# Kernel optimization log

Measured on AMD Instinct MI355X. Metric: run time of the kernel, lower is better.

Reference implementation:

```python
import math
import jax, jax.numpy as jnp
import numpy as np

H = 8  # num_heads


def setup_inputs() -> dict:
    key = jax.random.key(0)
    ks = jax.random.split(key, 9)
    B, N = 2, 4096
    Cc, C, Cs = 512, 512, 128  # in_channels, hidden_size, in_channels//4
    f = lambda k, shp: jax.random.normal(k, shp, dtype=jnp.float32) * 0.02
    return {
        "s": f(ks[0], (B, N, Cc)),
        "h": f(ks[1], (B, N, Cs)),
        "sh": f(ks[2], (B, N, C)),
        "temperature": jnp.full((H, 1, 1), 0.1, jnp.float32),
        "temperature2": jnp.full((H, 1, 1), 0.1, jnp.float32),
        "Wq_c": f(ks[3], (Cc, Cc)),
        "Wq_s": f(ks[4], (C, C)),
        "Wk_c": f(ks[5], (C, C)),
        "Wv_c": f(ks[6], (C, C)),
        "Wk_s": f(ks[7], (C, C)),
        "Wv_s": f(ks[8], (Cs, Cs)),
    }


def reference(s, h, sh, temperature, temperature2, Wq_c, Wq_s, Wk_c, Wv_c, Wk_s, Wv_s):
    B, N, C = sh.shape
    Cc = s.shape[2]
    Cs = h.shape[2]
    dc, d, ds = Cc // H, C // H, Cs // H

    # torch nn.Linear(bias=False): y = x @ W.T ; reshapes replicate torch's
    # direct reshape(B, H, N, d) layout (no (B,N,H,d)+transpose head split).
    q_c = (s @ Wq_c.T).reshape(B, H, N, dc).swapaxes(-1, -2)  # (B,H,dc,N)
    q_s = (sh @ Wq_s.T).reshape(B, H, N, d)
    k_c = (sh @ Wk_c.T).reshape(B, H, N, d)
    v_c = (sh @ Wv_c.T).reshape(B, H, N, d)
    k_s = (sh @ Wk_s.T).reshape(B, H, N, d)
    v_s = (h @ Wv_s.T).reshape(B, H, N, ds)

    # Channel branch: (B,H,dc,N) @ (B,H,N,d) -> (B,H,dc,d)
    attn_ca = (q_c @ k_c) / math.sqrt(d) * temperature
    attn_ca = jax.nn.softmax(attn_ca, axis=-1)
    x_ca = (attn_ca @ v_c.swapaxes(-2, -1)).reshape(B, N, Cc)  # (B,H,dc,N)->(B,N,Cc)

    # Spatial branch: (B,H,N,d) @ (B,H,d,N) -> (B,H,N,N)
    attn_sa = (q_s @ k_s.swapaxes(-2, -1)) / math.sqrt(d) * temperature2
    attn_sa = jax.nn.softmax(attn_sa, axis=-1)
    x_sa = (attn_sa @ v_s).reshape(B, N, Cs)  # (B,H,N,ds)->(B,N,Cs)

    return jnp.concatenate([x_ca, x_sa], axis=2)  # (B,N,Cc+Cs)
```

## Files before the change

### kernel.cpp

```cpp
#include <hip/hip_runtime.h>


typedef __attribute__((ext_vector_type(8))) __bf16 bf16x8;
typedef __attribute__((ext_vector_type(4))) __bf16 bf16x4;
typedef __attribute__((ext_vector_type(4))) float  f32x4;
typedef __attribute__((ext_vector_type(4))) short  s16x4;

#define LOG2E 1.44269504088896340736f

static __device__ __forceinline__ f32x4 mfma16(bf16x4 a, bf16x4 b, f32x4 c)
{
#if __has_builtin(__builtin_amdgcn_mfma_f32_16x16x16bf16_1k)
    union { bf16x4 h; s16x4 s; } ua, ub;
    ua.h = a; ub.h = b;
    return __builtin_amdgcn_mfma_f32_16x16x16bf16_1k(ua.s, ub.s, c, 0, 0, 0);
#elif __has_builtin(__builtin_amdgcn_mfma_f32_16x16x16_bf16)
    return __builtin_amdgcn_mfma_f32_16x16x16_bf16(a, b, c, 0, 0, 0);
#else
    asm("v_mfma_f32_16x16x16_bf16 %0, %1, %2, %0" : "+v"(c) : "v"(a), "v"(b));
    return c;
#endif
}

__global__ void detect_dtype(const unsigned* __restrict__ temp, int* __restrict__ flag)
{
    if (threadIdx.x == 0) {
        const unsigned w = temp[0];
        flag[0] = ((w >> 16) == (w & 0xffffu)) ? 1 : 0;
    }
}

struct ProjArgs {
    const void* X[6];
    const void* W[6];
    __bf16*     Y[6];
    int         K[6];
    int         yofs[7];
    int         ng;
};

__global__ __launch_bounds__(256) void proj_gemm(ProjArgs args,
                                                 const int* __restrict__ flag)
{
    __shared__ __align__(16) __bf16 As[128][72];
    __shared__ __align__(16) __bf16 Bs[128][72];
    const int bf = *flag;
    const int by = blockIdx.y;
    int g = 0;
    while (by >= args.yofs[g + 1]) ++g;
    const int n0 = (by - args.yofs[g]) * 128;
    const int N  = (args.yofs[g + 1] - args.yofs[g]) * 128;
    const int K  = args.K[g];
    const void* X = args.X[g];
    const void* W = args.W[g];
    __bf16*     Y = args.Y[g];

    const int m0 = blockIdx.x * 128;
    const int t = threadIdx.x;
    const int wave = t >> 6, lane = t & 63;
    const int wr = (wave >> 1) * 64, wc = (wave & 1) * 64;
    const int m16 = lane & 15, quad = lane >> 4;

    f32x4 acc[4][4];
#pragma unroll
    for (int i = 0; i < 4; ++i)
#pragma unroll
        for (int j = 0; j < 4; ++j) acc[i][j] = (f32x4){0.f, 0.f, 0.f, 0.f};

    if (bf) {
        const __bf16* Xb = (const __bf16*)X;
        const __bf16* Wb = (const __bf16*)W;
        bf16x8 pa[4], pb[4];
        auto load = [&](int k0) {
#pragma unroll
            for (int i = 0; i < 4; ++i) {
                const int idx = t + i * 256, row = idx >> 3, off = (idx & 7) * 8;
                pa[i] = *(const bf16x8*)(Xb + (size_t)(m0 + row) * K + k0 + off);
            }
#pragma unroll
            for (int i = 0; i < 4; ++i) {
                const int idx = t + i * 256, row = idx >> 3, off = (idx & 7) * 8;
                pb[i] = *(const bf16x8*)(Wb + (size_t)(n0 + row) * K + k0 + off);
            }
        };
        load(0);
        for (int k0 = 0; k0 < K; k0 += 64) {
            __syncthreads();
#pragma unroll
            for (int i = 0; i < 4; ++i) {
                const int idx = t + i * 256, row = idx >> 3, off = (idx & 7) * 8;
                *(bf16x8*)&As[row][off] = pa[i];
            }
#pragma unroll
            for (int i = 0; i < 4; ++i) {
                const int idx = t + i * 256, row = idx >> 3, off = (idx & 7) * 8;
                *(bf16x8*)&Bs[row][off] = pb[i];
            }
            __syncthreads();
            if (k0 + 64 < K) load(k0 + 64);
#pragma unroll
            for (int kc = 0; kc < 2; ++kc) {
                const int ko = kc * 32 + quad * 8;
                bf16x8 a[4], b[4];
#pragma unroll
                for (int i = 0; i < 4; ++i) a[i] = *(const bf16x8*)&As[wr + i * 16 + m16][ko];
#pragma unroll
                for (int j = 0; j < 4; ++j) b[j] = *(const bf16x8*)&Bs[wc + j * 16 + m16][ko];
#pragma unroll
                for (int i = 0; i < 4; ++i)
#pragma unroll
                    for (int j = 0; j < 4; ++j)
                        acc[i][j] = __builtin_amdgcn_mfma_f32_16x16x32_bf16(a[i], b[j], acc[i][j], 0, 0, 0);
            }
        }
    } else {
        const float* Xf = (const float*)X;
        const float* Wf = (const float*)W;
        f32x4 pa[8], pb[8];
        auto load = [&](int k0) {
#pragma unroll
            for (int i = 0; i < 8; ++i) {
                const int idx = t + i * 256, row = idx >> 4, c = (idx & 15) * 4;
                pa[i] = *(const f32x4*)(Xf + (size_t)(m0 + row) * K + k0 + c);
            }
#pragma unroll
            for (int i = 0; i < 8; ++i) {
                const int idx = t + i * 256, row = idx >> 4, c = (idx & 15) * 4;
                pb[i] = *(const f32x4*)(Wf + (size_t)(n0 + row) * K + k0 + c);
            }
        };
        load(0);
        for (int k0 = 0; k0 < K; k0 += 64) {
            __syncthreads();
#pragma unroll
            for (int i = 0; i < 8; ++i) {
                const int idx = t + i * 256, row = idx >> 4, c = (idx & 15) * 4;
                bf16x4 ha;
#pragma unroll
                for (int e = 0; e < 4; ++e) ha[e] = (__bf16)pa[i][e];
                *(bf16x4*)&As[row][c] = ha;
            }
#pragma unroll
            for (int i = 0; i < 8; ++i) {
                const int idx = t + i * 256, row = idx >> 4, c = (idx & 15) * 4;
                bf16x4 hb;
#pragma unroll
                for (int e = 0; e < 4; ++e) hb[e] = (__bf16)pb[i][e];
                *(bf16x4*)&Bs[row][c] = hb;
            }
            __syncthreads();
            if (k0 + 64 < K) load(k0 + 64);
#pragma unroll
            for (int kc = 0; kc < 2; ++kc) {
                const int ko = kc * 32 + quad * 8;
                bf16x8 a[4], b[4];
#pragma unroll
                for (int i = 0; i < 4; ++i) a[i] = *(const bf16x8*)&As[wr + i * 16 + m16][ko];
#pragma unroll
                for (int j = 0; j < 4; ++j) b[j] = *(const bf16x8*)&Bs[wc + j * 16 + m16][ko];
#pragma unroll
                for (int i = 0; i < 4; ++i)
#pragma unroll
                    for (int j = 0; j < 4; ++j)
                        acc[i][j] = __builtin_amdgcn_mfma_f32_16x16x32_bf16(a[i], b[j], acc[i][j], 0, 0, 0);
            }
        }
    }
#pragma unroll
    for (int i = 0; i < 4; ++i)
#pragma unroll
        for (int j = 0; j < 4; ++j)
#pragma unroll
            for (int r = 0; r < 4; ++r) {
                const int gm = m0 + wr + i * 16 + quad * 4 + r;
                const int gn = n0 + wc + j * 16 + m16;
                Y[(size_t)gm * N + gn] = (__bf16)acc[i][j][r];
            }
}

__global__ __launch_bounds__(256) void zero_f32(float* __restrict__ p, int n)
{
    const int i = blockIdx.x * 256 + threadIdx.x;
    if (i < n) p[i] = 0.f;
}

template <int ATOMIC>
__global__ __launch_bounds__(256) void chan_qk(const __bf16* __restrict__ Qc,
                                               const __bf16* __restrict__ Kc,
                                               float* __restrict__ S)
{
    __shared__ __align__(16) __bf16 Ql[128][72];
    __shared__ __align__(16) __bf16 Kl[128][72];
    const int bx = blockIdx.x;
    const int bh = bx >> 5, split = bx & 31;
    const int b = bh >> 3, hh = bh & 7;
    const int n0 = split * 128;
    const int t = threadIdx.x;
    const size_t base = ((size_t)b * 4096 + (size_t)hh * 512) * 512;

    for (int idx = t; idx < 1024; idx += 256) {
        const int row = idx >> 3, off = (idx & 7) * 8;
        *(bf16x8*)&Ql[row][off] = *(const bf16x8*)(Qc + base + (size_t)(n0 + row) * 64 + off);
        *(bf16x8*)&Kl[row][off] = *(const bf16x8*)(Kc + base + (size_t)(n0 + row) * 64 + off);
    }
    __syncthreads();

    const int ti = t >> 4, tj = t & 15;
    float acc[4][4];
#pragma unroll
    for (int r = 0; r < 4; ++r)
#pragma unroll
        for (int c = 0; c < 4; ++c) acc[r][c] = 0.f;

#pragma unroll 4
    for (int n = 0; n < 128; ++n) {
        bf16x4 qv = *(const bf16x4*)&Ql[n][ti * 4];
        bf16x4 kv = *(const bf16x4*)&Kl[n][tj * 4];
        float qf[4], kf[4];
#pragma unroll
        for (int x = 0; x < 4; ++x) { qf[x] = (float)qv[x]; kf[x] = (float)kv[x]; }
#pragma unroll
        for (int r = 0; r < 4; ++r)
#pragma unroll
            for (int c = 0; c < 4; ++c) acc[r][c] += qf[r] * kf[c];
    }
    if (ATOMIC) {
        float* Sb = S + (size_t)bh * 4096;
#pragma unroll
        for (int r = 0; r < 4; ++r)
#pragma unroll
            for (int c = 0; c < 4; ++c)
                atomicAdd(&Sb[(ti * 4 + r) * 64 + tj * 4 + c], acc[r][c]);
    } else {
        float* Sp = S + (size_t)bx * 4096;
#pragma unroll
        for (int r = 0; r < 4; ++r)
#pragma unroll
            for (int c = 0; c < 4; ++c)
                Sp[(ti * 4 + r) * 64 + tj * 4 + c] = acc[r][c];
    }
}

__global__ __launch_bounds__(256) void qk_reduce(const float* __restrict__ Spart,
                                                 float* __restrict__ S)
{
    const int tid = blockIdx.x * 256 + threadIdx.x;
    const int bh = tid >> 12, ij = tid & 4095;
    const float* p = Spart + (size_t)bh * 32 * 4096 + ij;
    float s = 0.f;
#pragma unroll
    for (int sp = 0; sp < 32; ++sp) s += p[(size_t)sp * 4096];
    S[(size_t)bh * 4096 + ij] = s;
}

__global__ __launch_bounds__(64) void chan_softmax(const float* __restrict__ S,
                                                   const void* __restrict__ temp,
                                                   __bf16* __restrict__ P,
                                                   const int* __restrict__ flag)
{
    const int bh = blockIdx.x;
    const int hh = bh & 7;
    const int i = threadIdx.x;
    const float tv = (*flag) ? (float)((const __bf16*)temp)[hh] : ((const float*)temp)[hh];
    const float scale = 0.125f * tv;
    const float* row = S + (size_t)bh * 4096 + (size_t)i * 64;
    float v[64];
    float mx = -1e30f;
#pragma unroll
    for (int j = 0; j < 64; ++j) { v[j] = row[j] * scale; mx = fmaxf(mx, v[j]); }
    float sum = 0.f;
#pragma unroll
    for (int j = 0; j < 64; ++j) { float e = __builtin_amdgcn_exp2f((v[j] - mx) * LOG2E); v[j] = e; sum += e; }
    const float inv = 1.f / sum;
    __bf16* prow = P + (size_t)bh * 4096 + (size_t)i * 64;
#pragma unroll
    for (int j = 0; j < 64; ++j) prow[j] = (__bf16)(v[j] * inv);
}

__global__ __launch_bounds__(256) void chan_av(const __bf16* __restrict__ P,
                                               const __bf16* __restrict__ Vc,
                                               void* __restrict__ out,
                                               const int* __restrict__ flag)
{
    const int bf = *flag;
    const int bx = blockIdx.x;
    const int bh = bx >> 6, ch = bx & 63;
    const int b = bh >> 3, hh = bh & 7;
    const int n0 = ch * 64;
    const int t = threadIdx.x, wave = t >> 6, lane = t & 63;
    const int m16 = lane & 15, quad = lane >> 4;
    const size_t base = ((size_t)b * 4096 + (size_t)hh * 512) * 512;
    const __bf16* Pb = P + (size_t)bh * 4096;

    bf16x8 a[2];
#pragma unroll
    for (int kc = 0; kc < 2; ++kc)
        a[kc] = *(const bf16x8*)(Pb + (wave * 16 + m16) * 64 + kc * 32 + quad * 8);

    f32x4 acc[4];
#pragma unroll
    for (int nt = 0; nt < 4; ++nt) {
        acc[nt] = (f32x4){0.f, 0.f, 0.f, 0.f};
        const int n = n0 + nt * 16 + m16;
        bf16x8 bv[2];
#pragma unroll
        for (int kc = 0; kc < 2; ++kc)
            bv[kc] = *(const bf16x8*)(Vc + base + (size_t)n * 64 + kc * 32 + quad * 8);
#pragma unroll
        for (int kc = 0; kc < 2; ++kc)
            acc[nt] = __builtin_amdgcn_mfma_f32_16x16x32_bf16(a[kc], bv[kc], acc[nt], 0, 0, 0);
    }

#pragma unroll
    for (int nt = 0; nt < 4; ++nt) {
        const int n = n0 + nt * 16 + m16;
#pragma unroll
        for (int r = 0; r < 4; ++r) {
            const int i = wave * 16 + quad * 4 + r;
            const size_t addr = (size_t)b * 2621440
                              + (size_t)(hh * 512 + i * 8 + (n >> 9)) * 640 + (n & 511);
            if (bf) ((__bf16*)out)[addr] = (__bf16)acc[nt][r];
            else    ((float*)out)[addr]  = acc[nt][r];
        }
    }
}

template <int PATH>
__global__ __launch_bounds__(512) void flash_sa(const __bf16* __restrict__ Qs,
                                                const __bf16* __restrict__ Ks,
                                                const __bf16* __restrict__ Vs,
                                                const void* __restrict__ temp2,
                                                void* __restrict__ out,
                                                float* __restrict__ po,
                                                float* __restrict__ pl,
                                                const int* __restrict__ flag)
{
    __shared__ __align__(16) __bf16 Kl[2][64][72];
    __shared__ __align__(16) __bf16 Vt[2][16][72];
    const int bf = *flag;
    const int bid = blockIdx.x;
    const int qt = bid & 15;
    const int bh = bid >> 4;
    const int b = bh >> 3, hh = bh & 7;
    const int nspl = gridDim.y;
    const int spl  = blockIdx.y;
    const int nkt  = 64 / nspl;
    const int kt0  = spl * nkt;
    const int t = threadIdx.x, wave = t >> 6, lane = t & 63;
    const int m16 = lane & 15, quad = lane >> 4;
    const size_t base  = ((size_t)b * 4096 + (size_t)hh * 512) * 512;
    const size_t vbase = ((size_t)b * 4096 + (size_t)hh * 512) * 128;
    const float tv = bf ? (float)((const __bf16*)temp2)[hh] : ((const float*)temp2)[hh];
    const float sl = 0.125f * tv * LOG2E;

    bf16x8 qa[2][2];
#pragma unroll
    for (int g = 0; g < 2; ++g) {
        const int qrow = qt * 256 + g * 128 + wave * 16 + m16;
#pragma unroll
        for (int kc = 0; kc < 2; ++kc) {
            bf16x8 raw = *(const bf16x8*)(Qs + base + (size_t)qrow * 64 + kc * 32 + quad * 8);
#pragma unroll
            for (int e = 0; e < 8; ++e) qa[g][kc][e] = (__bf16)((float)raw[e] * sl);
        }
    }

    bf16x4 ones;
#pragma unroll
    for (int e = 0; e < 4; ++e) ones[e] = (__bf16)1.0f;

    const int krow = t >> 3, koff = (t & 7) * 8;
    const bool vact = t < 256;
    const int vrow = t & 63, vcq = (t >> 6) & 3;
    bf16x8 pk;
    bf16x4 pv;
    auto pref = [&](int kt) {
        pk = *(const bf16x8*)(Ks + base + (size_t)(kt * 64 + krow) * 64 + koff);
        if (vact) pv = *(const bf16x4*)(Vs + vbase + (size_t)(kt * 64 + vrow) * 16 + vcq * 4);
    };
    auto stage = [&](int bi) {
        *(bf16x8*)&Kl[bi][krow][koff] = pk;
        if (vact) {
#pragma unroll
            for (int e = 0; e < 4; ++e) Vt[bi][vcq * 4 + e][vrow] = pv[e];
        }
    };

    pref(kt0);
    stage(0);
    pref(kt0 + 1);
    __syncthreads();

    f32x4 o[2]  = {(f32x4){0.f, 0.f, 0.f, 0.f}, (f32x4){0.f, 0.f, 0.f, 0.f}};
    f32x4 o2[2] = {(f32x4){0.f, 0.f, 0.f, 0.f}, (f32x4){0.f, 0.f, 0.f, 0.f}};

    for (int kk = 0; kk < nkt; ++kk) {
        const int cur = kk & 1;

        bf16x8 kb[4][2];
        bf16x4 vb16[4];
#pragma unroll
        for (int ct = 0; ct < 4; ++ct)
#pragma unroll
            for (int kc = 0; kc < 2; ++kc)
                kb[ct][kc] = *(const bf16x8*)&Kl[cur][ct * 16 + m16][kc * 32 + quad * 8];
#pragma unroll
        for (int ct = 0; ct < 4; ++ct)
            vb16[ct] = *(const bf16x4*)&Vt[cur][m16][ct * 16 + quad * 4];

        if (kk + 1 < nkt) stage(cur ^ 1);
        if (kk + 2 < nkt) pref(kt0 + kk + 2);

#pragma unroll
        for (int g = 0; g < 2; ++g) {
            f32x4 st[4];
#pragma unroll
            for (int ct = 0; ct < 4; ++ct) {
                st[ct] = (f32x4){0.f, 0.f, 0.f, 0.f};
#pragma unroll
                for (int kc = 0; kc < 2; ++kc)
                    st[ct] = __builtin_amdgcn_mfma_f32_16x16x32_bf16(kb[ct][kc], qa[g][kc], st[ct], 0, 0, 0);
            }
#pragma unroll
            for (int ct = 0; ct < 4; ++ct) {
                bf16x4 pe;
#pragma unroll
                for (int r = 0; r < 4; ++r)
                    pe[r] = (__bf16)__builtin_amdgcn_exp2f(st[ct][r]);
                o[g]  = mfma16(pe, vb16[ct], o[g]);
                o2[g] = mfma16(pe, ones,     o2[g]);
            }
        }
        __syncthreads();
    }

    asm volatile("s_nop 7\n\ts_nop 7");

    if (nspl == 1) {
#pragma unroll
        for (int g = 0; g < 2; ++g) {
#pragma unroll
            for (int r = 0; r < 4; ++r) {
                const int n = qt * 256 + g * 128 + wave * 16 + quad * 4 + r;
                const float val = o[g][r] / o2[g][r];
                const size_t addr = (size_t)b * 2621440
                                  + (size_t)(hh * 512 + (n >> 3)) * 640 + 512 + (n & 7) * 16 + m16;
                if (bf) ((__bf16*)out)[addr] = (__bf16)val;
                else    ((float*)out)[addr]  = val;
            }
        }
    } else {
#pragma unroll
        for (int g = 0; g < 2; ++g) {
#pragma unroll
            for (int r = 0; r < 4; ++r) {
                const int n = qt * 256 + g * 128 + wave * 16 + quad * 4 + r;
                const size_t rowi = ((size_t)spl * 16 + bh) * 4096 + n;
                po[rowi * 16 + m16] = o[g][r];
                if (m16 == 0) pl[rowi] = o2[g][r];
            }
        }
    }
}

__global__ __launch_bounds__(256) void flash_combine(const float* __restrict__ po,
                                                     const float* __restrict__ pl,
                                                     void* __restrict__ out,
                                                     const int* __restrict__ flag,
                                                     int nspl)
{
    const int bf = *flag;
    const int tid = blockIdx.x * 256 + threadIdx.x;
    const int bh = tid >> 12, n = tid & 4095;
    const int b = bh >> 3, hh = bh & 7;

    float acc[16];
#pragma unroll
    for (int c = 0; c < 16; ++c) acc[c] = 0.f;
    float l = 0.f;
    for (int sp = 0; sp < nspl; ++sp) {
        const size_t rowi = ((size_t)sp * 16 + bh) * 4096 + n;
        const f32x4* r = (const f32x4*)(po + rowi * 16);
#pragma unroll
        for (int q = 0; q < 4; ++q) {
            const f32x4 v = r[q];
#pragma unroll
            for (int e = 0; e < 4; ++e) acc[q * 4 + e] += v[e];
        }
        l += pl[rowi];
    }
    const float inv = 1.f / l;
    const size_t addr = (size_t)b * 2621440
                      + (size_t)(hh * 512 + (n >> 3)) * 640 + 512 + (n & 7) * 16;
    if (bf) {
#pragma unroll
        for (int c = 0; c < 16; ++c) ((__bf16*)out)[addr + c] = (__bf16)(acc[c] * inv);
    } else {
#pragma unroll
        for (int c = 0; c < 16; ++c) ((float*)out)[addr + c] = acc[c] * inv;
    }
}

extern "C" void kernel_launch(void* const* d_in, const int* in_sizes, int n_in,
                              void* d_out, int out_size, void* d_ws, size_t ws_size,
                              hipStream_t stream)
{
    const void* s    = d_in[0];
    const void* h_   = d_in[1];
    const void* sh   = d_in[2];
    const void* t1   = d_in[3];
    const void* t2   = d_in[4];
    const void* Wq_c = d_in[5];
    const void* Wq_s = d_in[6];
    const void* Wk_c = d_in[7];
    const void* Wv_c = d_in[8];
    const void* Wk_s = d_in[9];
    const void* Wv_s = d_in[10];

    const dim3 blk(256);
    const size_t PROJ = 4194304;

    const size_t WIDE_BYTES = 5 * PROJ * 2 + 1048576 * 2 + 65536 * 4 + 65536 * 2 + 256;

    if (ws_size >= WIDE_BYTES) {
        __bf16* qc = (__bf16*)d_ws;
        __bf16* kc = qc + PROJ;
        __bf16* vc = kc + PROJ;
        __bf16* qs = vc + PROJ;
        __bf16* ks = qs + PROJ;
        __bf16* vs = ks + PROJ;
        float*  Sb = (float*)(vs + 1048576);
        __bf16* Pb = (__bf16*)(Sb + 65536);
        int*  flag = (int*)(Pb + 65536);

        detect_dtype<<<dim3(1), dim3(64), 0, stream>>>((const unsigned*)t1, flag);

        ProjArgs pa{};
        const void* Xs[6] = {s, sh, sh, sh, sh, h_};
        const void* Ws[6] = {Wq_c, Wk_c, Wv_c, Wq_s, Wk_s, Wv_s};
        __bf16*     Ys[6] = {qc, kc, vc, qs, ks, vs};
        const int   Ks_[6] = {512, 512, 512, 512, 512, 128};
        const int   yt[6] = {4, 4, 4, 4, 4, 1};
        pa.ng = 6;
        int ofs = 0;
        for (int g = 0; g < 6; ++g) {
            pa.X[g] = Xs[g]; pa.W[g] = Ws[g]; pa.Y[g] = Ys[g]; pa.K[g] = Ks_[g];
            pa.yofs[g] = ofs; ofs += yt[g];
        }
        pa.yofs[6] = ofs;

        proj_gemm<<<dim3(64, 21), blk, 0, stream>>>(pa, flag);

        zero_f32<<<dim3(256), blk, 0, stream>>>(Sb, 65536);
        chan_qk<1><<<dim3(512), blk, 0, stream>>>(qc, kc, Sb);
        chan_softmax<<<dim3(16), dim3(64), 0, stream>>>(Sb, t1, Pb, flag);
        chan_av<<<dim3(1024), blk, 0, stream>>>(Pb, vc, d_out, flag);
        float* po = (float*)qc;
        float* pl = po + 4ull * 1048576;
        flash_sa<0><<<dim3(256, 4), dim3(512), 0, stream>>>(qs, ks, vs, t2, d_out, po, pl, flag);
        flash_combine<<<dim3(256), blk, 0, stream>>>(po, pl, d_out, flag, 4);
    } else {
        __bf16* A  = (__bf16*)d_ws;
        __bf16* Bf = A + PROJ;
        __bf16* D  = Bf + PROJ;
        float*  Sb = (float*)(D + 1048576);
        __bf16* Pb = (__bf16*)(Sb + 65536);
        int*  flag = (int*)(Pb + 65536);

        detect_dtype<<<dim3(1), dim3(64), 0, stream>>>((const unsigned*)t1, flag);

        auto mk2 = [&](const void* X0, const void* W0, __bf16* Y0, int K0, int t0,
                       const void* X1, const void* W1, __bf16* Y1, int K1, int t1_) {
            ProjArgs p{};
            p.ng = 2;
            p.X[0] = X0; p.W[0] = W0; p.Y[0] = Y0; p.K[0] = K0;
            p.X[1] = X1; p.W[1] = W1; p.Y[1] = Y1; p.K[1] = K1;
            p.yofs[0] = 0; p.yofs[1] = t0; p.yofs[2] = t0 + t1_;
            return p;
        };

        const size_t fb_end = (size_t)((char*)(flag + 1) - (char*)d_ws);
        const size_t pofs = (fb_end + 255) & ~(size_t)255;
        const size_t per_split = (1048576 + 65536) * 4;
        const size_t qk_bytes = 512ull * 4096 * 4;
        int nspl = 1;
        if (ws_size >= pofs + 4 * per_split)      nspl = 4;
        else if (ws_size >= pofs + 2 * per_split) nspl = 2;
        const bool qk_part = (ws_size >= pofs + qk_bytes);
        float* scratch = (float*)((char*)d_ws + pofs);

        ProjArgs p1 = mk2(s,  Wq_c, A,  512, 4, sh, Wk_c, Bf, 512, 4);
        proj_gemm<<<dim3(64, 8), blk, 0, stream>>>(p1, flag);
        if (qk_part) {
            chan_qk<0><<<dim3(512), blk, 0, stream>>>(A, Bf, scratch);
            qk_reduce<<<dim3(256), blk, 0, stream>>>(scratch, Sb);
        } else {
            zero_f32<<<dim3(256), blk, 0, stream>>>(Sb, 65536);
            chan_qk<1><<<dim3(512), blk, 0, stream>>>(A, Bf, Sb);
        }
        chan_softmax<<<dim3(16), dim3(64), 0, stream>>>(Sb, t1, Pb, flag);

        ProjArgs p2 = mk2(sh, Wv_c, A, 512, 4, sh, Wq_s, Bf, 512, 4);
        proj_gemm<<<dim3(64, 8), blk, 0, stream>>>(p2, flag);
        chan_av<<<dim3(1024), blk, 0, stream>>>(Pb, A, d_out, flag);

        ProjArgs p3 = mk2(sh, Wk_s, A, 512, 4, h_, Wv_s, D, 128, 1);
        proj_gemm<<<dim3(64, 5), blk, 0, stream>>>(p3, flag);

        float* po = scratch;
        float* pl = po + (size_t)nspl * 1048576;
        flash_sa<1><<<dim3(256, nspl), dim3(512), 0, stream>>>(Bf, A, D, t2, d_out, po, pl, flag);
        if (nspl > 1)
            flash_combine<<<dim3(256), blk, 0, stream>>>(po, pl, d_out, flag, nspl);
    }
}
```

Baseline: 246.7 us.

## Pre-transpose V_s in projection epilogue, fuse QK reduce into wave-parallel softmax

The projection GEMM epilogue for the K=128 group (V_s) now writes its output transposed per head into a channel-major layout. This lets flash_sa load V fragments straight from global memory instead of staging and transposing them through shared memory. The channel softmax is rewritten to give each row one wave, using shuffle reductions, across 256 blocks instead of 16, and it also sums the 32 split partials, which removes the separate qk_reduce launch. The risks are scattered, uncoalesced stores in the GEMM epilogue and V reads from global memory inside the flash loop with no prefetch.

```diff
diff --git a/kernel.cpp b/kernel.cpp
--- a/kernel.cpp
+++ b/kernel.cpp
@@ -166,16 +166,34 @@
             }
         }
     }
-#pragma unroll
-    for (int i = 0; i < 4; ++i)
-#pragma unroll
-        for (int j = 0; j < 4; ++j)
-#pragma unroll
-            for (int r = 0; r < 4; ++r) {
-                const int gm = m0 + wr + i * 16 + quad * 4 + r;
+    if (K == 128) {
+#pragma unroll
+        for (int i = 0; i < 4; ++i)
+#pragma unroll
+            for (int j = 0; j < 4; ++j) {
                 const int gn = n0 + wc + j * 16 + m16;
-                Y[(size_t)gm * N + gn] = (__bf16)acc[i][j][r];
-            }
+                const int c_ = gn & 15, cg = gn >> 4;
+#pragma unroll
+                for (int r = 0; r < 4; ++r) {
+                    const int gm = m0 + wr + i * 16 + quad * 4 + r;
+                    const int b_ = gm >> 12, n_ = gm & 4095;
+                    const int h_ = n_ >> 9;
+                    const int key = ((n_ & 511) << 3) | cg;
+                    Y[(((size_t)b_ * 8 + h_) * 16 + c_) * 4096 + key] = (__bf16)acc[i][j][r];
+                }
+            }
+    } else {
+#pragma unroll
+        for (int i = 0; i < 4; ++i)
+#pragma unroll
+            for (int j = 0; j < 4; ++j)
+#pragma unroll
+                for (int r = 0; r < 4; ++r) {
+                    const int gm = m0 + wr + i * 16 + quad * 4 + r;
+                    const int gn = n0 + wc + j * 16 + m16;
+                    Y[(size_t)gm * N + gn] = (__bf16)acc[i][j][r];
+                }
+    }
 }
 
 __global__ __launch_bounds__(256) void zero_f32(float* __restrict__ p, int n)
@@ -241,40 +259,37 @@
     }
 }
 
-__global__ __launch_bounds__(256) void qk_reduce(const float* __restrict__ Spart,
-                                                 float* __restrict__ S)
-{
-    const int tid = blockIdx.x * 256 + threadIdx.x;
-    const int bh = tid >> 12, ij = tid & 4095;
-    const float* p = Spart + (size_t)bh * 32 * 4096 + ij;
-    float s = 0.f;
-#pragma unroll
-    for (int sp = 0; sp < 32; ++sp) s += p[(size_t)sp * 4096];
-    S[(size_t)bh * 4096 + ij] = s;
-}
-
-__global__ __launch_bounds__(64) void chan_softmax(const float* __restrict__ S,
-                                                   const void* __restrict__ temp,
-                                                   __bf16* __restrict__ P,
-                                                   const int* __restrict__ flag)
-{
-    const int bh = blockIdx.x;
+template <int NSPLIT>
+__global__ __launch_bounds__(256) void chan_softmax(const float* __restrict__ S,
+                                                    const void* __restrict__ temp,
+                                                    __bf16* __restrict__ P,
+                                                    const int* __restrict__ flag)
+{
+    const int row = blockIdx.x * 4 + (threadIdx.x >> 6);
+    const int bh = row >> 6, i = row & 63;
     const int hh = bh & 7;
-    const int i = threadIdx.x;
+    const int j = threadIdx.x & 63;
     const float tv = (*flag) ? (float)((const __bf16*)temp)[hh] : ((const float*)temp)[hh];
     const float scale = 0.125f * tv;
-    const float* row = S + (size_t)bh * 4096 + (size_t)i * 64;
-    float v[64];
-    float mx = -1e30f;
-#pragma unroll
-    for (int j = 0; j < 64; ++j) { v[j] = row[j] * scale; mx = fmaxf(mx, v[j]); }
-    float sum = 0.f;
-#pragma unroll
-    for (int j = 0; j < 64; ++j) { float e = __builtin_amdgcn_exp2f((v[j] - mx) * LOG2E); v[j] = e; sum += e; }
-    const float inv = 1.f / sum;
-    __bf16* prow = P + (size_t)bh * 4096 + (size_t)i * 64;
-#pragma unroll
-    for (int j = 0; j < 64; ++j) prow[j] = (__bf16)(v[j] * inv);
+
+    float v;
+    if (NSPLIT > 1) {
+        const float* p = S + ((size_t)bh * NSPLIT) * 4096 + (size_t)i * 64 + j;
+        float s = 0.f;
+#pragma unroll
+        for (int sp = 0; sp < NSPLIT; ++sp) s += p[(size_t)sp * 4096];
+        v = s * scale;
+    } else {
+        v = S[(size_t)bh * 4096 + (size_t)i * 64 + j] * scale;
+    }
+    float mx = v;
+#pragma unroll
+    for (int d = 1; d < 64; d <<= 1) mx = fmaxf(mx, __shfl_xor(mx, d, 64));
+    const float e = __builtin_amdgcn_exp2f((v - mx) * LOG2E);
+    float sum = e;
+#pragma unroll
+    for (int d = 1; d < 64; d <<= 1) sum += __shfl_xor(sum, d, 64);
+    P[(size_t)bh * 4096 + (size_t)i * 64 + j] = (__bf16)(e / sum);
 }
 
 __global__ __launch_bounds__(256) void chan_av(const __bf16* __restrict__ P,
@@ -336,7 +351,6 @@
                                                 const int* __restrict__ flag)
 {
     __shared__ __align__(16) __bf16 Kl[2][64][72];
-    __shared__ __align__(16) __bf16 Vt[2][16][72];
     const int bf = *flag;
     const int bid = blockIdx.x;
     const int qt = bid & 15;
@@ -348,11 +362,12 @@
     const int kt0  = spl * nkt;
     const int t = threadIdx.x, wave = t >> 6, lane = t & 63;
     const int m16 = lane & 15, quad = lane >> 4;
-    const size_t base  = ((size_t)b * 4096 + (size_t)hh * 512) * 512;
-    const size_t vbase = ((size_t)b * 4096 + (size_t)hh * 512) * 128;
+    const size_t base = ((size_t)b * 4096 + (size_t)hh * 512) * 512;
     const float tv = bf ? (float)((const __bf16*)temp2)[hh] : ((const float*)temp2)[hh];
     const float sl = 0.125f * tv * LOG2E;
 
+    const __bf16* Vh = Vs + ((size_t)bh * 16 + m16) * 4096;
+
     bf16x8 qa[2][2];
 #pragma unroll
     for (int g = 0; g < 2; ++g) {
@@ -370,20 +385,12 @@
     for (int e = 0; e < 4; ++e) ones[e] = (__bf16)1.0f;
 
     const int krow = t >> 3, koff = (t & 7) * 8;
-    const bool vact = t < 256;
-    const int vrow = t & 63, vcq = (t >> 6) & 3;
     bf16x8 pk;
-    bf16x4 pv;
     auto pref = [&](int kt) {
         pk = *(const bf16x8*)(Ks + base + (size_t)(kt * 64 + krow) * 64 + koff);
-        if (vact) pv = *(const bf16x4*)(Vs + vbase + (size_t)(kt * 64 + vrow) * 16 + vcq * 4);
     };
     auto stage = [&](int bi) {
         *(bf16x8*)&Kl[bi][krow][koff] = pk;
-        if (vact) {
-#pragma unroll
-            for (int e = 0; e < 4; ++e) Vt[bi][vcq * 4 + e][vrow] = pv[e];
-        }
     };
 
     pref(kt0);
@@ -396,17 +403,19 @@
 
     for (int kk = 0; kk < nkt; ++kk) {
         const int cur = kk & 1;
+        const int kta = kt0 + kk;
+
+        bf16x4 vb16[4];
+#pragma unroll
+        for (int ct = 0; ct < 4; ++ct)
+            vb16[ct] = *(const bf16x4*)(Vh + (size_t)kta * 64 + ct * 16 + quad * 4);
 
         bf16x8 kb[4][2];
-        bf16x4 vb16[4];
 #pragma unroll
         for (int ct = 0; ct < 4; ++ct)
 #pragma unroll
             for (int kc = 0; kc < 2; ++kc)
                 kb[ct][kc] = *(const bf16x8*)&Kl[cur][ct * 16 + m16][kc * 32 + quad * 8];
-#pragma unroll
-        for (int ct = 0; ct < 4; ++ct)
-            vb16[ct] = *(const bf16x4*)&Vt[cur][m16][ct * 16 + quad * 4];
 
         if (kk + 1 < nkt) stage(cur ^ 1);
         if (kk + 2 < nkt) pref(kt0 + kk + 2);
@@ -553,7 +562,7 @@
 
         zero_f32<<<dim3(256), blk, 0, stream>>>(Sb, 65536);
         chan_qk<1><<<dim3(512), blk, 0, stream>>>(qc, kc, Sb);
-        chan_softmax<<<dim3(16), dim3(64), 0, stream>>>(Sb, t1, Pb, flag);
+        chan_softmax<1><<<dim3(256), blk, 0, stream>>>(Sb, t1, Pb, flag);
         chan_av<<<dim3(1024), blk, 0, stream>>>(Pb, vc, d_out, flag);
         float* po = (float*)qc;
         float* pl = po + 4ull * 1048576;
@@ -593,12 +602,12 @@
         proj_gemm<<<dim3(64, 8), blk, 0, stream>>>(p1, flag);
         if (qk_part) {
             chan_qk<0><<<dim3(512), blk, 0, stream>>>(A, Bf, scratch);
-            qk_reduce<<<dim3(256), blk, 0, stream>>>(scratch, Sb);
+            chan_softmax<32><<<dim3(256), blk, 0, stream>>>(scratch, t1, Pb, flag);
         } else {
             zero_f32<<<dim3(256), blk, 0, stream>>>(Sb, 65536);
             chan_qk<1><<<dim3(512), blk, 0, stream>>>(A, Bf, Sb);
-        }
-        chan_softmax<<<dim3(16), dim3(64), 0, stream>>>(Sb, t1, Pb, flag);
+            chan_softmax<1><<<dim3(256), blk, 0, stream>>>(Sb, t1, Pb, flag);
+        }
 
         ProjArgs p2 = mk2(sh, Wv_c, A, 512, 4, sh, Wq_s, Bf, 512, 4);
         proj_gemm<<<dim3(64, 8), blk, 0, stream>>>(p2, flag);
```

Result: slower. 266.3 us (+8.0%).
